# Kernel optimization log

Hardware: AMD Instinct MI355X
Metric: run time of the kernel (lower is better)

Reference implementation:

```python
import jax, jax.numpy as jnp
import numpy as np

B, N, ESM_DIM, D, K = 256, 100000, 1280, 512, 8
ATT_TAU = 1.0
NEG_INF_FILL = -10000.0
EPS = 1e-6


def _l2norm(x, axis=-1):
    return x / jnp.linalg.norm(x, axis=axis, keepdims=True).clip(1e-12)


def setup_inputs() -> dict:
    key = jax.random.key(0)
    ks = jax.random.split(key, 8)
    index_emb = _l2norm(jax.random.normal(ks[0], (N, ESM_DIM), jnp.float32))
    return {
        "query_esm_pooled": jax.random.normal(ks[1], (B, ESM_DIM), jnp.float32),
        "model_embs": jax.random.normal(ks[2], (B, D), jnp.float32),
        "index_emb": index_emb,
        "index_labels": jax.random.randint(ks[3], (N,), 0, 2, jnp.int64),
        "exclude_idx": jax.random.randint(ks[4], (B,), 0, N, jnp.int64),
        "proj_W": jax.random.normal(ks[5], (ESM_DIM, D), jnp.float32) * 0.02,
        "proj_b": jnp.zeros((D,), jnp.float32),
        "clf_W": jax.random.normal(ks[6], (2 * D, 2), jnp.float32) * 0.02,
        "clf_b": jnp.zeros((2,), jnp.float32),
    }


def reference(query_esm_pooled, model_embs, index_emb, index_labels, exclude_idx,
              proj_W, proj_b, clf_W, clf_b):
    # esm_dim != model_emb_dim -> use ESM-pooled queries, project neighbors
    Q = _l2norm(query_esm_pooled)                       # [B, E]
    sims = Q @ index_emb.T                              # [B, N] cosine (index pre-normalized)
    sims = sims.at[jnp.arange(B), exclude_idx].set(NEG_INF_FILL)
    _, topk = jax.lax.top_k(sims, K)                    # [B, K]

    neigh_raw = index_emb[topk]                         # [B, K, E]
    neigh_lbl = index_labels[topk]                      # [B, K]
    neigh_proj = neigh_raw @ proj_W + proj_b            # [B, K, D]

    # tiny cross-attention: query = model_embs, keys/values = neighbors
    scale = 1.0 / (jnp.sqrt(jnp.float32(D)) * ATT_TAU)
    att = jax.nn.softmax(jnp.einsum('bd,bkd->bk', model_embs, neigh_proj) * scale, axis=-1)
    z_neigh = jnp.einsum('bk,bkd->bd', att, neigh_proj)  # [B, D]

    logits_retr = jnp.concatenate([model_embs, z_neigh], axis=1) @ clf_W + clf_b  # [B, 2]

    # prototypes (detached, matching torch.no_grad)
    mask_pos = (neigh_lbl == 1).astype(jnp.float32)     # [B, K]
    mask_neg = (neigh_lbl == 0).astype(jnp.float32)
    pos_proto = jnp.einsum('bk,bkd->bd', mask_pos, neigh_proj) / (mask_pos.sum(1, keepdims=True) + EPS)
    neg_proto = jnp.einsum('bk,bkd->bd', mask_neg, neigh_proj) / (mask_neg.sum(1, keepdims=True) + EPS)
    pos_proto = jax.lax.stop_gradient(pos_proto)
    neg_proto = jax.lax.stop_gradient(neg_proto)

    retr_align_loss = jnp.mean((model_embs - pos_proto) ** 2) - 0.5 * jnp.mean((model_embs - neg_proto) ** 2)
    return logits_retr, retr_align_loss
```

## Files before the change

### kernel.cpp

```cpp
#include <hip/hip_runtime.h>
#include <math.h>

#define B_SZ 256
#define N_SZ 100000
#define E_SZ 1280
#define D_SZ 512

#define NCH 1563

typedef __attribute__((ext_vector_type(8))) short s8v;
typedef __attribute__((ext_vector_type(4))) float f32x4;

__device__ __forceinline__ unsigned short f2bf(float f) {
  unsigned int u = __float_as_uint(f);
  u += 0x7fffu + ((u >> 16) & 1u);
  return (unsigned short)(u >> 16);
}
__device__ __forceinline__ unsigned int pack2(float a, float b) {
  return (unsigned)f2bf(a) | ((unsigned)f2bf(b) << 16);
}

#define TOP8_UPDATE(v_, i_)                                                 \
  if ((v_) > minv) {                                                        \
    _Pragma("unroll")                                                       \
    for (int s_ = 0; s_ < 8; ++s_)                                          \
      if (s_ == mins) { bv[s_] = (v_); bi[s_] = (i_); }                     \
    minv = bv[0]; mins = 0;                                                 \
    _Pragma("unroll")                                                       \
    for (int s_ = 1; s_ < 8; ++s_)                                          \
      if (bv[s_] < minv) { minv = bv[s_]; mins = s_; }                      \
  }

__global__ __launch_bounds__(256) void k_normq(const float* __restrict__ q,
                                               unsigned short* __restrict__ qn) {
  __shared__ float red[4];
  int row = blockIdx.x, t = threadIdx.x;
  const float* src = q + (size_t)row * E_SZ;
  float x[5];
  float ss = 0.f;
#pragma unroll
  for (int i = 0; i < 5; ++i) { x[i] = src[t + 256 * i]; ss += x[i] * x[i]; }
#pragma unroll
  for (int o = 32; o > 0; o >>= 1) ss += __shfl_down(ss, o, 64);
  if ((t & 63) == 0) red[t >> 6] = ss;
  __syncthreads();
  float nrm = sqrtf(red[0] + red[1] + red[2] + red[3]);
  nrm = fmaxf(nrm, 1e-12f);
  float inv = 1.0f / nrm;
  unsigned short* dst = qn + (size_t)row * E_SZ;
#pragma unroll
  for (int i = 0; i < 5; ++i) dst[t + 256 * i] = f2bf(x[i] * inv);
}

__global__ __launch_bounds__(256) void k_wt(const float* __restrict__ W,
                                            unsigned short* __restrict__ Wt) {
  __shared__ float T[64][65];
  const int kb = blockIdx.x * 64;
  const int nb = blockIdx.y * 64;
  const int t = threadIdx.x;
#pragma unroll
  for (int i = 0; i < 16; ++i) {
    int kr = i * 4 + (t >> 6);
    T[kr][t & 63] = W[(size_t)(kb + kr) * D_SZ + nb + (t & 63)];
  }
  __syncthreads();
  const int n = t >> 2, ks = (t & 3) * 16;
  unsigned int ow[8];
#pragma unroll
  for (int j = 0; j < 8; ++j)
    ow[j] = (unsigned)f2bf(T[ks + 2 * j][n]) |
            ((unsigned)f2bf(T[ks + 2 * j + 1][n]) << 16);
  unsigned short* dst = Wt + (size_t)(nb + n) * E_SZ + kb + ks;
  *(uint4*)dst = make_uint4(ow[0], ow[1], ow[2], ow[3]);
  *(uint4*)(dst + 8) = make_uint4(ow[4], ow[5], ow[6], ow[7]);
}

__global__ __launch_bounds__(256) void k_sims_topk(
    const unsigned short* __restrict__ qn, const float* __restrict__ emb,
    const int* __restrict__ excl, float* __restrict__ cval) {
  __shared__ __align__(16) char lds[40960];
  const int t = threadIdx.x;
  const int l = t & 63, w = t >> 6;
  const int r15 = l & 15, g = l >> 4;
  const int jbase = blockIdx.x * 64;

  const int myq = (w << 6) + l;
  const int ex = excl[myq];

  f32x4 acc[4][4];
#pragma unroll
  for (int i = 0; i < 4; ++i)
#pragma unroll
    for (int j = 0; j < 4; ++j) acc[i][j] = (f32x4)0.f;

  const int ar = t >> 2;
  const int akc = t & 3;
  const int brow = t >> 2;
  const int bkc = t & 3;
  const bool bval = (jbase + brow) < N_SZ;
  const float* bptr = emb + (size_t)(jbase + brow) * E_SZ + bkc * 8;

  char* A0 = lds;
  char* A1 = lds + 16384;
  char* B0 = lds + 32768;
  char* B1 = lds + 36864;

  int awoff[4];
#pragma unroll
  for (int i = 0; i < 4; ++i) {
    int row = i * 64 + ar;
    awoff[i] = row * 64 + (((akc + (row >> 1)) & 3) << 4);
  }
  const int bwoff = brow * 64 + (((bkc + (brow >> 1)) & 3) << 4);

  int afoff[4], bfoff[4];
#pragma unroll
  for (int mq = 0; mq < 4; ++mq) {
    int row = (w << 6) + 16 * mq + r15;
    afoff[mq] = row * 64 + (((g + (row >> 1)) & 3) << 4);
  }
#pragma unroll
  for (int nj = 0; nj < 4; ++nj) {
    int row = 16 * nj + r15;
    bfoff[nj] = row * 64 + (((g + (row >> 1)) & 3) << 4);
  }

  s8v a0[4], a1[4];
  float4 b0[2], b1[2];

#define LOADA(set_, kt_)                                                     \
  { _Pragma("unroll") for (int i_ = 0; i_ < 4; ++i_)                         \
      set_[i_] = *(const s8v*)(qn + (size_t)(i_ * 64 + ar) * E_SZ + (kt_) +  \
                               akc * 8); }
#define LOADB(set_, kt_)                                                     \
  { if (bval) { set_[0] = *(const float4*)(bptr + (kt_));                    \
                set_[1] = *(const float4*)(bptr + (kt_) + 4); }              \
    else { set_[0] = make_float4(0.f,0.f,0.f,0.f);                           \
           set_[1] = make_float4(0.f,0.f,0.f,0.f); } }
#define WRA(set_, base_)                                                     \
  { _Pragma("unroll") for (int i_ = 0; i_ < 4; ++i_)                         \
      *(s8v*)((base_) + awoff[i_]) = set_[i_]; }
#define WRB(set_, base_)                                                     \
  { uint4 p_;                                                                \
    p_.x = pack2(set_[0].x, set_[0].y); p_.y = pack2(set_[0].z, set_[0].w);  \
    p_.z = pack2(set_[1].x, set_[1].y); p_.w = pack2(set_[1].z, set_[1].w);  \
    *(uint4*)((base_) + bwoff) = p_; }
#define COMPUTE(Ab_, Bb_)                                                    \
  { s8v af_[4];                                                              \
    _Pragma("unroll") for (int mq_ = 0; mq_ < 4; ++mq_)                      \
      af_[mq_] = *(const s8v*)((Ab_) + afoff[mq_]);                          \
    _Pragma("unroll") for (int nj_ = 0; nj_ < 4; ++nj_) {                    \
      s8v bf_ = *(const s8v*)((Bb_) + bfoff[nj_]);                           \
      _Pragma("unroll") for (int mq_ = 0; mq_ < 4; ++mq_)                    \
        acc[mq_][nj_] = __builtin_amdgcn_mfma_f32_16x16x32_bf16(             \
            af_[mq_], bf_, acc[mq_][nj_], 0, 0, 0);                          \
    } }
#define FENCE_BAR                                                            \
  { asm volatile("s_waitcnt lgkmcnt(0)" ::: "memory");                       \
    __builtin_amdgcn_s_barrier(); }

  LOADA(a0, 0); LOADB(b0, 0);
  LOADA(a1, 32); LOADB(b1, 32);
  WRA(a0, A0); WRB(b0, B0);
  FENCE_BAR;

  for (int s = 0; s < 38; s += 2) {
    LOADA(a0, (s + 2) * 32); LOADB(b0, (s + 2) * 32);
    COMPUTE(A0, B0);
    WRA(a1, A1); WRB(b1, B1);
    FENCE_BAR;
    LOADA(a1, (s + 3) * 32); LOADB(b1, (s + 3) * 32);
    COMPUTE(A1, B1);
    WRA(a0, A0); WRB(b0, B0);
    FENCE_BAR;
  }
  COMPUTE(A0, B0);
  WRA(a1, A1); WRB(b1, B1);
  FENCE_BAR;
  COMPUTE(A1, B1);
  FENCE_BAR;

  float* Sbuf = (float*)(lds + (w & 1) * 16896);
  for (int ph = 0; ph < 2; ++ph) {
    if ((w >> 1) == ph) {
#pragma unroll
      for (int mq = 0; mq < 4; ++mq)
#pragma unroll
        for (int nj = 0; nj < 4; ++nj)
#pragma unroll
          for (int r = 0; r < 4; ++r)
            Sbuf[(16 * mq + 4 * g + r) * 66 + 16 * nj + r15] = acc[mq][nj][r];
      float bv[8]; int bi[8];
#pragma unroll
      for (int s = 0; s < 8; ++s) { bv[s] = -1e30f; bi[s] = 0; }
      float minv = -1e30f; int mins = 0;
      const float* Srow = Sbuf + l * 66;
      for (int c = 0; c < 64; ++c) {
        int gj = jbase + c;
        float v = Srow[c];
        if (gj < N_SZ && gj != ex) { TOP8_UPDATE(v, gj); }
      }
      float* vdst = cval + (size_t)blockIdx.x * 4096 + myq * 8;
      *(float4*)vdst = make_float4(bv[0], bv[1], bv[2], bv[3]);
      *(float4*)(vdst + 4) = make_float4(bv[4], bv[5], bv[6], bv[7]);
      int* idst = (int*)(cval + (size_t)blockIdx.x * 4096 + 2048) + myq * 8;
      *(int4*)idst = make_int4(bi[0], bi[1], bi[2], bi[3]);
      *(int4*)(idst + 4) = make_int4(bi[4], bi[5], bi[6], bi[7]);
    }
    FENCE_BAR;
  }
#undef LOADA
#undef LOADB
#undef WRA
#undef WRB
#undef COMPUTE
#undef FENCE_BAR
}

__global__ __launch_bounds__(256) void k_merge(const float* __restrict__ cval,
                                               int* __restrict__ topk) {
  __shared__ float sv[2048];
  __shared__ int si[2048];
  const int q = blockIdx.x, t = threadIdx.x;
  float bv[8]; int bi[8];
#pragma unroll
  for (int s = 0; s < 8; ++s) { bv[s] = -1e30f; bi[s] = 0; }
  float minv = -1e30f; int mins = 0;
  for (int c = t; c < NCH; c += 256) {
    const float* vp = cval + (size_t)c * 4096 + q * 8;
    const int* ip = (const int*)(cval + (size_t)c * 4096 + 2048) + q * 8;
    float4 v0 = *(const float4*)vp, v1 = *(const float4*)(vp + 4);
    int4 i0 = *(const int4*)ip, i1 = *(const int4*)(ip + 4);
    float va[8] = {v0.x, v0.y, v0.z, v0.w, v1.x, v1.y, v1.z, v1.w};
    int ia[8] = {i0.x, i0.y, i0.z, i0.w, i1.x, i1.y, i1.z, i1.w};
#pragma unroll
    for (int s = 0; s < 8; ++s) {
      float v = va[s]; int ix = ia[s];
      TOP8_UPDATE(v, ix);
    }
  }
#pragma unroll
  for (int s = 0; s < 8; ++s) { sv[t * 8 + s] = bv[s]; si[t * 8 + s] = bi[s]; }
  __syncthreads();
  if (t < 64) {
    for (int rr = 1; rr < 4; ++rr) {
      int r = t + rr * 64;
#pragma unroll
      for (int s = 0; s < 8; ++s) {
        float v = sv[r * 8 + s]; int ix = si[r * 8 + s];
        TOP8_UPDATE(v, ix);
      }
    }
#pragma unroll
    for (int s = 0; s < 8; ++s) { sv[t * 8 + s] = bv[s]; si[t * 8 + s] = bi[s]; }
  }
  __syncthreads();
  if (t < 8) {
    for (int rr = 1; rr < 8; ++rr) {
      int r = t + rr * 8;
#pragma unroll
      for (int s = 0; s < 8; ++s) {
        float v = sv[r * 8 + s]; int ix = si[r * 8 + s];
        TOP8_UPDATE(v, ix);
      }
    }
#pragma unroll
    for (int s = 0; s < 8; ++s) { sv[t * 8 + s] = bv[s]; si[t * 8 + s] = bi[s]; }
  }
  __syncthreads();
  if (t == 0) {
    for (int r = 1; r < 8; ++r) {
#pragma unroll
      for (int s = 0; s < 8; ++s) {
        float v = sv[r * 8 + s]; int ix = si[r * 8 + s];
        TOP8_UPDATE(v, ix);
      }
    }
#pragma unroll
    for (int s = 0; s < 8; ++s) topk[q * 8 + s] = bi[s];
  }
}

__global__ __launch_bounds__(256) void k_proj(
    const float* __restrict__ emb, const int* __restrict__ topk,
    const unsigned short* __restrict__ Wt, const float* __restrict__ bias,
    float* __restrict__ nproj) {
  __shared__ __align__(16) char lds[65536];
  const int t = threadIdx.x, l = t & 63, w = t >> 6;
  const int r15 = l & 15, g = l >> 4;
  const int wm = w >> 1, wn = w & 1;
  const int r0 = blockIdx.x * 128, n0 = blockIdx.y * 128;
  const int sr = t >> 3, kc = t & 7;

  int grow[4];
#pragma unroll
  for (int i = 0; i < 4; ++i) grow[i] = topk[r0 + i * 32 + sr];

  int woff[4];
#pragma unroll
  for (int i = 0; i < 4; ++i) {
    int row = i * 32 + sr;
    woff[i] = row * 128 + (((kc + (row & 7)) & 7) << 4);
  }
  int afoff[2][4], bfoff[2][4];
#pragma unroll
  for (int h = 0; h < 2; ++h) {
#pragma unroll
    for (int qq = 0; qq < 4; ++qq) {
      int rowa = 64 * wm + 16 * qq + r15;
      afoff[h][qq] = rowa * 128 + ((((h << 2) + g + (rowa & 7)) & 7) << 4);
      int rowb = 64 * wn + 16 * qq + r15;
      bfoff[h][qq] = rowb * 128 + ((((h << 2) + g + (rowb & 7)) & 7) << 4);
    }
  }

  f32x4 acc[4][4];
#pragma unroll
  for (int i = 0; i < 4; ++i)
#pragma unroll
    for (int j = 0; j < 4; ++j) acc[i][j] = (f32x4)0.f;

  float4 aset[4][2];
  s8v bset[4];

#define PLOADA(kt_)                                                          \
  { _Pragma("unroll") for (int i_ = 0; i_ < 4; ++i_) {                       \
      const float* s_ = emb + (size_t)grow[i_] * E_SZ + (kt_) + kc * 8;      \
      aset[i_][0] = *(const float4*)s_;                                      \
      aset[i_][1] = *(const float4*)(s_ + 4); } }
#define PLOADB(kt_)                                                          \
  { _Pragma("unroll") for (int i_ = 0; i_ < 4; ++i_)                         \
      bset[i_] = *(const s8v*)(Wt + (size_t)(n0 + i_ * 32 + sr) * E_SZ +     \
                               (kt_) + kc * 8); }
#define PWR(bA_, bB_)                                                        \
  { _Pragma("unroll") for (int i_ = 0; i_ < 4; ++i_) {                       \
      uint4 p_;                                                              \
      p_.x = pack2(aset[i_][0].x, aset[i_][0].y);                            \
      p_.y = pack2(aset[i_][0].z, aset[i_][0].w);                            \
      p_.z = pack2(aset[i_][1].x, aset[i_][1].y);                            \
      p_.w = pack2(aset[i_][1].z, aset[i_][1].w);                            \
      *(uint4*)((bA_) + woff[i_]) = p_;                                      \
      *(s8v*)((bB_) + woff[i_]) = bset[i_]; } }
#define PCOMP(bA_, bB_)                                                      \
  { _Pragma("unroll") for (int h_ = 0; h_ < 2; ++h_) {                       \
      s8v af_[4], bf_[4];                                                    \
      _Pragma("unroll") for (int q_ = 0; q_ < 4; ++q_) {                     \
        af_[q_] = *(const s8v*)((bA_) + afoff[h_][q_]);                      \
        bf_[q_] = *(const s8v*)((bB_) + bfoff[h_][q_]); }                    \
      _Pragma("unroll") for (int nj_ = 0; nj_ < 4; ++nj_)                    \
        _Pragma("unroll") for (int mq_ = 0; mq_ < 4; ++mq_)                  \
          acc[mq_][nj_] = __builtin_amdgcn_mfma_f32_16x16x32_bf16(           \
              af_[mq_], bf_[nj_], acc[mq_][nj_], 0, 0, 0); } }

  PLOADA(0); PLOADB(0);
  PWR(lds, lds + 32768);
  __syncthreads();
  for (int s = 0; s < 20; ++s) {
    char* cA = lds + (s & 1) * 16384;
    char* cB = lds + 32768 + (s & 1) * 16384;
    char* nA = lds + ((s + 1) & 1) * 16384;
    char* nB = lds + 32768 + ((s + 1) & 1) * 16384;
    if (s + 1 < 20) { PLOADA((s + 1) * 64); PLOADB((s + 1) * 64); }
    PCOMP(cA, cB);
    if (s + 1 < 20) { PWR(nA, nB); }
    __syncthreads();
  }
#pragma unroll
  for (int nj = 0; nj < 4; ++nj) {
    int n = n0 + 64 * wn + 16 * nj + r15;
    float bn = bias[n];
#pragma unroll
    for (int mq = 0; mq < 4; ++mq) {
      int m = r0 + 64 * wm + 16 * mq + 4 * g;
#pragma unroll
      for (int r = 0; r < 4; ++r)
        nproj[(size_t)(m + r) * D_SZ + n] = acc[mq][nj][r] + bn;
    }
  }
#undef PLOADA
#undef PLOADB
#undef PWR
#undef PCOMP
}

__global__ __launch_bounds__(256) void k_attn(
    const float* __restrict__ model, const float* __restrict__ proj,
    const int* __restrict__ topk, const int* __restrict__ labels,
    const float* __restrict__ clfW, const float* __restrict__ clfb,
    float* __restrict__ out, float* __restrict__ lossp) {
  __shared__ float P[8 * 512];
  __shared__ float red[4];
  int b = blockIdx.x, t = threadIdx.x;
  const float* src = proj + (size_t)b * 8 * 512;
#pragma unroll
  for (int i = 0; i < 4; ++i) {
    int o = i * 1024 + t * 4;
    *(float4*)&P[o] = *(const float4*)&src[o];
  }
  __syncthreads();
  float m0 = model[b * 512 + t], m1 = model[b * 512 + 256 + t];

  float sc[8];
#pragma unroll
  for (int k = 0; k < 8; ++k) {
    float p = m0 * P[k * 512 + t] + m1 * P[k * 512 + 256 + t];
#pragma unroll
    for (int o = 32; o > 0; o >>= 1) p += __shfl_down(p, o, 64);
    if ((t & 63) == 0) red[t >> 6] = p;
    __syncthreads();
    sc[k] = red[0] + red[1] + red[2] + red[3];
    __syncthreads();
  }
  const float scale = 0.04419417382415922f;
  float mx = -1e30f;
  float s_[8];
#pragma unroll
  for (int k = 0; k < 8; ++k) { s_[k] = sc[k] * scale; mx = fmaxf(mx, s_[k]); }
  float den = 0.f, att[8];
#pragma unroll
  for (int k = 0; k < 8; ++k) { att[k] = expf(s_[k] - mx); den += att[k]; }
  float iden = 1.0f / den;
#pragma unroll
  for (int k = 0; k < 8; ++k) att[k] *= iden;

  float z0 = 0.f, z1 = 0.f;
#pragma unroll
  for (int k = 0; k < 8; ++k) {
    z0 = fmaf(att[k], P[k * 512 + t], z0);
    z1 = fmaf(att[k], P[k * 512 + 256 + t], z1);
  }
#pragma unroll
  for (int c = 0; c < 2; ++c) {
    float lp = m0 * clfW[t * 2 + c] + m1 * clfW[(t + 256) * 2 + c] +
               z0 * clfW[(512 + t) * 2 + c] + z1 * clfW[(768 + t) * 2 + c];
#pragma unroll
    for (int o = 32; o > 0; o >>= 1) lp += __shfl_down(lp, o, 64);
    if ((t & 63) == 0) red[t >> 6] = lp;
    __syncthreads();
    if (t == 0) out[b * 2 + c] = red[0] + red[1] + red[2] + red[3] + clfb[c];
    __syncthreads();
  }
  float cp = 0.f, cn = 0.f;
  float p0 = 0.f, p1 = 0.f, n0 = 0.f, n1 = 0.f;
#pragma unroll
  for (int k = 0; k < 8; ++k) {
    int lb = labels[topk[b * 8 + k]];
    float mp = (lb == 1) ? 1.f : 0.f;
    float mn = (lb == 0) ? 1.f : 0.f;
    cp += mp; cn += mn;
    p0 = fmaf(mp, P[k * 512 + t], p0);
    p1 = fmaf(mp, P[k * 512 + 256 + t], p1);
    n0 = fmaf(mn, P[k * 512 + t], n0);
    n1 = fmaf(mn, P[k * 512 + 256 + t], n1);
  }
  float icp = 1.0f / (cp + 1e-6f), icn = 1.0f / (cn + 1e-6f);
  p0 *= icp; p1 *= icp; n0 *= icn; n1 *= icn;
  float lq = (m0 - p0) * (m0 - p0) + (m1 - p1) * (m1 - p1) -
             0.5f * ((m0 - n0) * (m0 - n0) + (m1 - n1) * (m1 - n1));
#pragma unroll
  for (int o = 32; o > 0; o >>= 1) lq += __shfl_down(lq, o, 64);
  if ((t & 63) == 0) red[t >> 6] = lq;
  __syncthreads();
  if (t == 0) lossp[b] = red[0] + red[1] + red[2] + red[3];
}

__global__ __launch_bounds__(256) void k_loss(const float* __restrict__ lossp,
                                              float* __restrict__ out) {
  __shared__ float red[4];
  int t = threadIdx.x;
  float v = lossp[t];
#pragma unroll
  for (int o = 32; o > 0; o >>= 1) v += __shfl_down(v, o, 64);
  if ((t & 63) == 0) red[t >> 6] = v;
  __syncthreads();
  if (t == 0)
    out[512] = (red[0] + red[1] + red[2] + red[3]) * (1.0f / (256.0f * 512.0f));
}

extern "C" void kernel_launch(void* const* d_in, const int* in_sizes, int n_in,
                              void* d_out, int out_size, void* d_ws,
                              size_t ws_size, hipStream_t stream) {
  (void)in_sizes; (void)n_in; (void)out_size; (void)ws_size;
  const float* q      = (const float*)d_in[0];
  const float* model  = (const float*)d_in[1];
  const float* emb    = (const float*)d_in[2];
  const int*   labels = (const int*)d_in[3];
  const int*   excl   = (const int*)d_in[4];
  const float* projW  = (const float*)d_in[5];
  const float* projb  = (const float*)d_in[6];
  const float* clfW   = (const float*)d_in[7];
  const float* clfb   = (const float*)d_in[8];
  float* out = (float*)d_out;

  char* ws = (char*)d_ws;
  unsigned short* qn = (unsigned short*)ws;
  unsigned short* Wt = (unsigned short*)(ws + 655360);
  float* cval  = (float*)(ws + 1966080);
  int*   topk  = (int*)(ws + 27574272);
  float* nproj = (float*)(ws + 27582464);
  float* lossp = (float*)(ws + 31776768);

  k_normq<<<256, 256, 0, stream>>>(q, qn);
  k_wt<<<dim3(20, 8), 256, 0, stream>>>(projW, Wt);
  k_sims_topk<<<NCH, 256, 0, stream>>>(qn, emb, excl, cval);
  k_merge<<<256, 256, 0, stream>>>(cval, topk);
  k_proj<<<dim3(16, 4), 256, 0, stream>>>(emb, topk, Wt, projb, nproj);
  k_attn<<<256, 256, 0, stream>>>(model, nproj, topk, labels, clfW, clfb, out, lossp);
  k_loss<<<1, 256, 0, stream>>>(lossp, out);
}
```

Before: 390.4 us.

## Stage query tiles via direct global-to-LDS loads and rework sims pipeline

Query tiles for the sims GEMM now go straight from global memory into LDS with global_load_lds, replacing the register round trip and explicit LDS stores. The pipeline is rebuilt around vmcnt-based waits so loads stay in flight across barriers, with an XOR swizzle for the LDS layout. Out-of-range index rows are clamped instead of branched, and the score buffer row pitch drops from 66 to 65. The aim is lower VGPR pressure and fewer LDS write instructions, but the hand-written waitcnt counts must match how the compiler orders the loads, which is fragile.

```diff
diff --git a/kernel.cpp b/kernel.cpp
--- a/kernel.cpp
+++ b/kernel.cpp
@@ -18,6 +18,12 @@
 }
 __device__ __forceinline__ unsigned int pack2(float a, float b) {
   return (unsigned)f2bf(a) | ((unsigned)f2bf(b) << 16);
+}
+
+__device__ __forceinline__ void gload16(const void* g, void* l) {
+  __builtin_amdgcn_global_load_lds(
+      (const __attribute__((address_space(1))) void*)g,
+      (__attribute__((address_space(3))) void*)l, 16, 0, 0);
 }
 
 #define TOP8_UPDATE(v_, i_)                                                 \
@@ -83,7 +89,6 @@
   const int l = t & 63, w = t >> 6;
   const int r15 = l & 15, g = l >> 4;
   const int jbase = blockIdx.x * 64;
-
   const int myq = (w << 6) + l;
   const int ex = excl[myq];
 
@@ -93,108 +98,86 @@
 #pragma unroll
     for (int j = 0; j < 4; ++j) acc[i][j] = (f32x4)0.f;
 
-  const int ar = t >> 2;
-  const int akc = t & 3;
-  const int brow = t >> 2;
-  const int bkc = t & 3;
-  const bool bval = (jbase + brow) < N_SZ;
-  const float* bptr = emb + (size_t)(jbase + brow) * E_SZ + bkc * 8;
-
-  char* A0 = lds;
-  char* A1 = lds + 16384;
-  char* B0 = lds + 32768;
-  char* B1 = lds + 36864;
-
-  int awoff[4];
-#pragma unroll
-  for (int i = 0; i < 4; ++i) {
-    int row = i * 64 + ar;
-    awoff[i] = row * 64 + (((akc + (row >> 1)) & 3) << 4);
-  }
-  const int bwoff = brow * 64 + (((bkc + (brow >> 1)) & 3) << 4);
-
+  const int chunk = (t & 3) ^ ((t >> 3) & 3);
+  const unsigned short* aSrc0 = qn + (size_t)(t >> 2) * E_SZ + chunk * 8;
+  const int grow = min(jbase + (t >> 2), N_SZ - 1);
+  const float* bSrc = emb + (size_t)grow * E_SZ + chunk * 8;
+  const int bwr = t * 16;
+
+  const int fsw = ((g ^ ((r15 >> 1) & 3)) << 4);
   int afoff[4], bfoff[4];
 #pragma unroll
-  for (int mq = 0; mq < 4; ++mq) {
-    int row = (w << 6) + 16 * mq + r15;
-    afoff[mq] = row * 64 + (((g + (row >> 1)) & 3) << 4);
-  }
-#pragma unroll
-  for (int nj = 0; nj < 4; ++nj) {
-    int row = 16 * nj + r15;
-    bfoff[nj] = row * 64 + (((g + (row >> 1)) & 3) << 4);
-  }
-
-  s8v a0[4], a1[4];
-  float4 b0[2], b1[2];
-
-#define LOADA(set_, kt_)                                                     \
+  for (int mq = 0; mq < 4; ++mq)
+    afoff[mq] = ((w << 6) + mq * 16 + r15) * 64 + fsw;
+#pragma unroll
+  for (int nj = 0; nj < 4; ++nj)
+    bfoff[nj] = (nj * 16 + r15) * 64 + fsw;
+
+  float4 bw0[2], bw1[2];
+
+#define STAGEA(kt_, aoff_)                                                   \
   { _Pragma("unroll") for (int i_ = 0; i_ < 4; ++i_)                         \
-      set_[i_] = *(const s8v*)(qn + (size_t)(i_ * 64 + ar) * E_SZ + (kt_) +  \
-                               akc * 8); }
-#define LOADB(set_, kt_)                                                     \
-  { if (bval) { set_[0] = *(const float4*)(bptr + (kt_));                    \
-                set_[1] = *(const float4*)(bptr + (kt_) + 4); }              \
-    else { set_[0] = make_float4(0.f,0.f,0.f,0.f);                           \
-           set_[1] = make_float4(0.f,0.f,0.f,0.f); } }
-#define WRA(set_, base_)                                                     \
-  { _Pragma("unroll") for (int i_ = 0; i_ < 4; ++i_)                         \
-      *(s8v*)((base_) + awoff[i_]) = set_[i_]; }
-#define WRB(set_, base_)                                                     \
+      gload16(aSrc0 + (size_t)i_ * (64 * E_SZ) + (kt_),                      \
+              lds + (aoff_) + i_ * 4096 + w * 1024); }
+#define LOADB(br_, kt_)                                                      \
+  { br_[0] = *(const float4*)(bSrc + (kt_));                                 \
+    br_[1] = *(const float4*)(bSrc + (kt_) + 4); }
+#define CVTWR(br_, boff_)                                                    \
   { uint4 p_;                                                                \
-    p_.x = pack2(set_[0].x, set_[0].y); p_.y = pack2(set_[0].z, set_[0].w);  \
-    p_.z = pack2(set_[1].x, set_[1].y); p_.w = pack2(set_[1].z, set_[1].w);  \
-    *(uint4*)((base_) + bwoff) = p_; }
-#define COMPUTE(Ab_, Bb_)                                                    \
+    p_.x = pack2(br_[0].x, br_[0].y); p_.y = pack2(br_[0].z, br_[0].w);      \
+    p_.z = pack2(br_[1].x, br_[1].y); p_.w = pack2(br_[1].z, br_[1].w);      \
+    *(uint4*)(lds + (boff_) + bwr) = p_; }
+#define COMPUTE(aoff_, boff_)                                                \
   { s8v af_[4];                                                              \
     _Pragma("unroll") for (int mq_ = 0; mq_ < 4; ++mq_)                      \
-      af_[mq_] = *(const s8v*)((Ab_) + afoff[mq_]);                          \
+      af_[mq_] = *(const s8v*)(lds + (aoff_) + afoff[mq_]);                  \
     _Pragma("unroll") for (int nj_ = 0; nj_ < 4; ++nj_) {                    \
-      s8v bf_ = *(const s8v*)((Bb_) + bfoff[nj_]);                           \
+      s8v bf_ = *(const s8v*)(lds + (boff_) + bfoff[nj_]);                   \
       _Pragma("unroll") for (int mq_ = 0; mq_ < 4; ++mq_)                    \
         acc[mq_][nj_] = __builtin_amdgcn_mfma_f32_16x16x32_bf16(             \
             af_[mq_], bf_, acc[mq_][nj_], 0, 0, 0);                          \
     } }
-#define FENCE_BAR                                                            \
-  { asm volatile("s_waitcnt lgkmcnt(0)" ::: "memory");                       \
+#define FENCE2                                                               \
+  { asm volatile("s_waitcnt vmcnt(2) lgkmcnt(0)" ::: "memory");              \
     __builtin_amdgcn_s_barrier(); }
-
-  LOADA(a0, 0); LOADB(b0, 0);
-  LOADA(a1, 32); LOADB(b1, 32);
-  WRA(a0, A0); WRB(b0, B0);
-  FENCE_BAR;
-
-  for (int s = 0; s < 38; s += 2) {
-    LOADA(a0, (s + 2) * 32); LOADB(b0, (s + 2) * 32);
-    COMPUTE(A0, B0);
-    WRA(a1, A1); WRB(b1, B1);
-    FENCE_BAR;
-    LOADA(a1, (s + 3) * 32); LOADB(b1, (s + 3) * 32);
-    COMPUTE(A1, B1);
-    WRA(a0, A0); WRB(b0, B0);
-    FENCE_BAR;
-  }
-  COMPUTE(A0, B0);
-  WRA(a1, A1); WRB(b1, B1);
-  FENCE_BAR;
-  COMPUTE(A1, B1);
-  FENCE_BAR;
-
-  float* Sbuf = (float*)(lds + (w & 1) * 16896);
+#define FENCE0                                                               \
+  { asm volatile("s_waitcnt vmcnt(0) lgkmcnt(0)" ::: "memory");              \
+    __builtin_amdgcn_s_barrier(); }
+
+  STAGEA(0, 0);
+  LOADB(bw0, 0);
+  LOADB(bw1, 32);
+  CVTWR(bw0, 32768);
+  FENCE2;
+
+  for (int s = 0; s < 40; s += 2) {
+    STAGEA((s + 1) * 32, 16384);
+    if (s + 2 < 40) LOADB(bw0, (s + 2) * 32);
+    COMPUTE(0, 32768);
+    CVTWR(bw1, 36864);
+    if (s + 2 < 40) { FENCE2; } else { FENCE0; }
+    if (s + 2 < 40) STAGEA((s + 2) * 32, 0);
+    if (s + 3 < 40) LOADB(bw1, (s + 3) * 32);
+    COMPUTE(16384, 36864);
+    if (s + 2 < 40) CVTWR(bw0, 32768);
+    if (s + 3 < 40) { FENCE2; } else { FENCE0; }
+  }
+
   for (int ph = 0; ph < 2; ++ph) {
     if ((w >> 1) == ph) {
+      float* Sbuf = (float*)(lds + (w & 1) * 16640);
 #pragma unroll
       for (int mq = 0; mq < 4; ++mq)
 #pragma unroll
         for (int nj = 0; nj < 4; ++nj)
 #pragma unroll
           for (int r = 0; r < 4; ++r)
-            Sbuf[(16 * mq + 4 * g + r) * 66 + 16 * nj + r15] = acc[mq][nj][r];
+            Sbuf[(16 * mq + 4 * g + r) * 65 + 16 * nj + r15] = acc[mq][nj][r];
       float bv[8]; int bi[8];
 #pragma unroll
       for (int s = 0; s < 8; ++s) { bv[s] = -1e30f; bi[s] = 0; }
       float minv = -1e30f; int mins = 0;
-      const float* Srow = Sbuf + l * 66;
+      const float* Srow = Sbuf + l * 65;
       for (int c = 0; c < 64; ++c) {
         int gj = jbase + c;
         float v = Srow[c];
@@ -207,14 +190,14 @@
       *(int4*)idst = make_int4(bi[0], bi[1], bi[2], bi[3]);
       *(int4*)(idst + 4) = make_int4(bi[4], bi[5], bi[6], bi[7]);
     }
-    FENCE_BAR;
-  }
-#undef LOADA
+    __syncthreads();
+  }
+#undef STAGEA
 #undef LOADB
-#undef WRA
-#undef WRB
+#undef CVTWR
 #undef COMPUTE
-#undef FENCE_BAR
+#undef FENCE2
+#undef FENCE0
 }
 
 __global__ __launch_bounds__(256) void k_merge(const float* __restrict__ cval,
```

New measurement: 412.1 us. 5.5% more time.
